# Optimization experiments

Hardware: AMD Instinct MI355X
Metric: run time of the kernel (lower is better)

The kernel has to match this reference:

```python
import jax, jax.numpy as jnp
import numpy as np

DN = ('NCHW', 'OIHW', 'NCHW')
PAD1 = [(1, 1), (1, 1)]


def conv3x3(x, w):
    return jax.lax.conv_general_dilated(x, w, window_strides=(1, 1), padding=PAD1, dimension_numbers=DN)


def setup_inputs() -> dict:
    key = jax.random.key(0)
    ks = jax.random.split(key, 5)
    B, C, H, W = 8, 256, 56, 56
    return {
        'x': jax.random.normal(ks[0], (B, C, H, W), jnp.float32),
        'weight': jax.random.normal(ks[1], (C, C, 3, 3), jnp.float32) * 0.05,
        'A_w': jax.random.normal(ks[2], (1, C, 3, 3), jnp.float32),
        'se_w1': jax.random.normal(ks[3], (16, C, 3, 3), jnp.float32) * 0.02,
        'se_w2': jax.random.normal(ks[4], (1, 16, 3, 3), jnp.float32) * 0.1,
    }


def reference(x, weight, A_w, se_w1, se_w2):
    # weight = weight * A_w (A_w broadcasts over the output-channel dim)
    w = weight * A_w  # [C, C, 3, 3]
    # SE-style spatial attention map A: [B, 1, H, W]
    a = jax.nn.sigmoid(conv3x3(jax.nn.relu(conv3x3(x, se_w1)), se_w2))
    # Torch: unfold(x) * A, then matmul with flattened weight. Since A
    # broadcasts across the C*9 patch dim, this equals conv2d(x, w) * A.
    out = conv3x3(x, w) * a  # [B, C, H, W]
    return out
```

## Files before the change

kernel.cpp:

```cpp
#include <hip/hip_runtime.h>


typedef unsigned short u16;
typedef __bf16 bf16x8 __attribute__((ext_vector_type(8)));
typedef unsigned short us8 __attribute__((ext_vector_type(8)));
typedef unsigned short us4v __attribute__((ext_vector_type(4)));
typedef float f32x4 __attribute__((ext_vector_type(4)));
typedef float f4v __attribute__((ext_vector_type(4)));

#define HP 58
#define HW 3136

__device__ __forceinline__ u16 f2bf(float f) {
  unsigned u = __float_as_uint(f);
  u = (u + 0x7fffu + ((u >> 16) & 1u)) >> 16;
  return (u16)u;
}
__device__ __forceinline__ float bf2f(u16 v) {
  return __uint_as_float(((unsigned)v) << 16);
}

__device__ __forceinline__ void gload16(const u16* g, u16* l) {
  __builtin_amdgcn_global_load_lds((const __attribute__((address_space(1))) void*)g,
                                   (__attribute__((address_space(3))) void*)l,
                                   16, 0, 0);
}

__global__ void k_prep(const float* __restrict__ weight, const float* __restrict__ A_w,
                       const float* __restrict__ se_w1, u16* __restrict__ wb,
                       u16* __restrict__ w1b) {
  int idx = blockIdx.x * 256 + threadIdx.x;
  if (idx < 589824) {
    int tap = idx >> 16; int rem = idx & 65535; int o = rem >> 8; int c = rem & 255;
    wb[idx] = f2bf(weight[(o * 256 + c) * 9 + tap] * A_w[c * 9 + tap]);
  } else if (idx < 589824 + 36864) {
    int j = idx - 589824;
    int tap = j >> 12; int rem = j & 4095; int o = rem >> 8; int c = rem & 255;
    w1b[j] = f2bf(se_w1[(o * 256 + c) * 9 + tap]);
  }
}

__global__ __launch_bounds__(256) void k_transform(const float* __restrict__ x,
                                                   u16* __restrict__ xp) {
  __shared__ __align__(16) u16 trans[56 * 72];
  const int t = threadIdx.x;
  const int h = blockIdx.x;
  const int b = blockIdx.y;
  for (int cc = 0; cc < 4; ++cc) {
    const int c0 = cc * 64;
#pragma unroll
    for (int i = 0; i < 4; ++i) {
      int idx = t + 256 * i;
      if (idx < 896) {
        int ci = idx / 14, s = idx % 14;
        f4v v = *(const f4v*)(x + ((size_t)(b * 256 + c0 + ci)) * HW + h * 56 + s * 4);
#pragma unroll
        for (int j = 0; j < 4; ++j) trans[(s * 4 + j) * 72 + ci] = f2bf(v[j]);
      }
    }
    __syncthreads();
#pragma unroll
    for (int i = 0; i < 2; ++i) {
      int idx = t + 256 * i;
      if (idx < 448) {
        int w = idx >> 3, seg = idx & 7;
        us8 v = *(const us8*)&trans[w * 72 + seg * 8];
        *(us8*)(xp + ((size_t)((b * HP + h + 1) * HP + (w + 1))) * 256 + c0 + seg * 8) = v;
      }
    }
    __syncthreads();
  }
}

__global__ __launch_bounds__(256) void k_se1(const u16* __restrict__ xp,
                                             const u16* __restrict__ w1b,
                                             u16* __restrict__ se1p) {
  __shared__ __align__(16) u16 Alds[144 * 8 * 8];
  __shared__ __align__(16) u16 slab[2080 * 8];
  const int t = threadIdx.x;
  const int lane = t & 63;
  const int wv = t >> 6;
  const int l15 = lane & 15, lg = lane >> 4;
  const int h0 = blockIdx.x * 2;
  const int b = blockIdx.y;

  f32x4 acc[2];
  f32x4 z = {0.f, 0.f, 0.f, 0.f};
  acc[0] = z; acc[1] = z;

  for (int cc = 0; cc < 4; ++cc) {
    const int c0 = cc * 64;
    __syncthreads();
    for (int idx = t; idx < 1152; idx += 256) {
      int row = idx >> 3, seg = idx & 7;
      us8 v = *(const us8*)(w1b + ((size_t)row * 256 + c0 + seg * 8));
      *(us8*)&Alds[(row * 8 + (seg ^ (row & 7))) * 8] = v;
    }
#pragma unroll
    for (int i = 0; i < 8; ++i) {
      int s_lin = wv * 512 + i * 64 + lane;
      int r = s_lin >> 9, col = (s_lin >> 3) & 63, seg = s_lin & 7;
      const u16* src = xp + ((size_t)((b * HP + h0 + r) * HP + col)) * 256 + c0 +
                       ((seg ^ (col & 7)) * 8);
      gload16(src, &slab[(wv * 512 + i * 64) * 8]);
    }
    __syncthreads();
    for (int dh = 0; dh < 3; ++dh) {
      for (int dw = 0; dw < 3; ++dw) {
        const int tap = dh * 3 + dw;
#pragma unroll
        for (int kk = 0; kk < 2; ++kk) {
          int arow = tap * 16 + l15;
          bf16x8 af = *(const bf16x8*)&Alds[(arow * 8 + ((kk * 4 + lg) ^ (arow & 7))) * 8];
#pragma unroll
          for (int nt = 0; nt < 2; ++nt) {
            int p = wv * 32 + nt * 16 + l15;
            int rr = (p >> 6) + dh, col = (p & 63) + dw;
            bf16x8 bfr = *(const bf16x8*)&slab[((rr * 64 + col) * 8 + ((kk * 4 + lg) ^ (col & 7))) * 8];
            acc[nt] = __builtin_amdgcn_mfma_f32_16x16x32_bf16(af, bfr, acc[nt], 0, 0, 0);
          }
        }
      }
    }
  }
#pragma unroll
  for (int nt = 0; nt < 2; ++nt) {
    int p = wv * 32 + nt * 16 + l15;
    int r = p >> 6, w = p & 63;
    if (w < 56) {
      us4v pk;
#pragma unroll
      for (int reg = 0; reg < 4; ++reg) {
        float v = acc[nt][reg];
        v = v > 0.f ? v : 0.f;
        pk[reg] = f2bf(v);
      }
      *(us4v*)(se1p + ((size_t)((b * HP + h0 + r + 1) * HP + (w + 1))) * 16 + lg * 4) = pk;
    }
  }
}

__global__ __launch_bounds__(256) void k_se2(const u16* __restrict__ se1p,
                                             const float* __restrict__ se_w2,
                                             float* __restrict__ amap) {
  __shared__ float w2s[144];
  const int t = threadIdx.x;
  for (int i = t; i < 144; i += 256) w2s[i] = se_w2[i];
  __syncthreads();
  int gid = blockIdx.x * 256 + t;
  int pix = gid >> 1, half = gid & 1;
  int b = pix / HW, p = pix % HW, h = p / 56, w = p % 56;
  float s = 0.f;
  for (int dh = 0; dh < 3; ++dh) {
#pragma unroll
    for (int dw = 0; dw < 3; ++dw) {
      const u16* src = se1p + ((size_t)((b * HP + h + dh) * HP + (w + dw))) * 16 + half * 8;
      us8 v = *(const us8*)src;
      int tap = dh * 3 + dw;
#pragma unroll
      for (int ci = 0; ci < 8; ++ci) s += bf2f(v[ci]) * w2s[(half * 8 + ci) * 9 + tap];
    }
  }
  s += __shfl_xor(s, 1);
  if (half == 0) amap[pix] = 1.f / (1.f + expf(-s));
}

__global__ __launch_bounds__(256) void k_main(const u16* __restrict__ xp,
                                              const u16* __restrict__ wb,
                                              const float* __restrict__ amap,
                                              float* __restrict__ out) {
  __shared__ __align__(16) u16 Alds[2][8192];
  __shared__ __align__(16) u16 Blds[2][8192];
  const int t = threadIdx.x;
  const int lane = t & 63;
  const int wid = t >> 6;
  const int wm = wid >> 1;
  const int wn = wid & 1;
  const int l15 = lane & 15, lg = lane >> 4;
  const int lrow = lane >> 3, lseg = lane & 7;
  const int mbase = blockIdx.x * 128;
  const int h0 = blockIdx.y * 2;
  const int b = blockIdx.z;

  f32x4 acc[4][4];
  f32x4 z = {0.f, 0.f, 0.f, 0.f};
#pragma unroll
  for (int mt = 0; mt < 4; ++mt)
#pragma unroll
    for (int nt = 0; nt < 4; ++nt) acc[mt][nt] = z;

  auto stage = [&](int buf, int it) {
    const int tap = it >> 2, cc = it & 3;
    const int dh = tap / 3, dw = tap % 3;
    const int c0 = cc * 64;
#pragma unroll
    for (int i = 0; i < 4; ++i) {
      int li = wid * 4 + i;
      int row = li * 8 + lrow;
      const u16* srcA = wb + ((size_t)(tap * 256 + mbase + row)) * 256 + c0 +
                        ((lseg ^ (row & 7)) * 8);
      gload16(srcA, &Alds[buf][li * 512]);
      int r = row >> 6, w = row & 63;
      const u16* srcB = xp +
                        ((size_t)((b * HP + h0 + r + dh) * HP + (w + dw))) * 256 + c0 +
                        ((lseg ^ (row & 7)) * 8);
      gload16(srcB, &Blds[buf][li * 512]);
    }
  };

  stage(0, 0);
#pragma unroll 2
  for (int it = 0; it < 36; ++it) {
    const int cur = it & 1;
    if (it < 35) {
      stage(cur ^ 1, it + 1);
      asm volatile("s_waitcnt vmcnt(8)" ::: "memory");
    } else {
      asm volatile("s_waitcnt vmcnt(0)" ::: "memory");
    }
    __builtin_amdgcn_s_barrier();
    __builtin_amdgcn_sched_barrier(0);
#pragma unroll
    for (int kk = 0; kk < 2; ++kk) {
      bf16x8 af[4], bfr[4];
#pragma unroll
      for (int mt = 0; mt < 4; ++mt) {
        int row = wm * 64 + mt * 16 + l15;
        af[mt] = *(const bf16x8*)&Alds[cur][row * 64 + (((kk * 4 + lg) ^ (row & 7)) * 8)];
      }
#pragma unroll
      for (int nt = 0; nt < 4; ++nt) {
        int p = wn * 64 + nt * 16 + l15;
        bfr[nt] = *(const bf16x8*)&Blds[cur][p * 64 + (((kk * 4 + lg) ^ (p & 7)) * 8)];
      }
#pragma unroll
      for (int mt = 0; mt < 4; ++mt)
#pragma unroll
        for (int nt = 0; nt < 4; ++nt)
          acc[mt][nt] = __builtin_amdgcn_mfma_f32_16x16x32_bf16(af[mt], bfr[nt], acc[mt][nt], 0, 0, 0);
    }
    __builtin_amdgcn_sched_barrier(0);
    __builtin_amdgcn_s_barrier();
  }
#pragma unroll
  for (int nt = 0; nt < 4; ++nt) {
    int n = wn * 64 + nt * 16 + l15;
    int r = n >> 6, w = n & 63;
    if (w < 56) {
      float av = amap[(b * 56 + h0 + r) * 56 + w];
#pragma unroll
      for (int mt = 0; mt < 4; ++mt) {
        int obase = mbase + wm * 64 + mt * 16 + lg * 4;
#pragma unroll
        for (int reg = 0; reg < 4; ++reg) {
          out[((size_t)(b * 256 + obase + reg) * 56 + h0 + r) * 56 + w] = acc[mt][nt][reg] * av;
        }
      }
    }
  }
}

extern "C" void kernel_launch(void* const* d_in, const int* in_sizes, int n_in,
                              void* d_out, int out_size, void* d_ws, size_t ws_size,
                              hipStream_t stream) {
  const float* x      = (const float*)d_in[0];
  const float* weight = (const float*)d_in[1];
  const float* A_w    = (const float*)d_in[2];
  const float* se_w1  = (const float*)d_in[3];
  const float* se_w2  = (const float*)d_in[4];
  float* out = (float*)d_out;

  char* ws = (char*)d_ws;
  u16* xp     = (u16*)ws;
  u16* se1p   = (u16*)(ws + 13778944);
  u16* wb     = (u16*)(ws + 14640128);
  u16* w1b    = (u16*)(ws + 15819776);
  float* amap = (float*)(ws + 15893504);

  hipMemsetAsync(ws, 0, 14640128, stream);
  k_prep<<<dim3((589824 + 36864 + 255) / 256), dim3(256), 0, stream>>>(weight, A_w, se_w1, wb, w1b);
  k_transform<<<dim3(56, 8), dim3(256), 0, stream>>>(x, xp);
  k_se1<<<dim3(28, 8), dim3(256), 0, stream>>>(xp, w1b, se1p);
  k_se2<<<dim3(196), dim3(256), 0, stream>>>(se1p, se_w2, amap);
  k_main<<<dim3(2, 28, 8), dim3(256), 0, stream>>>(xp, wb, amap, out);
}
```

Measured before the change: 154.3 us.

## Fuse prep kernels, stage input slab once per channel chunk, fold SE2 into main

New measurement: 171.4 us. 1.11x slower.

```diff
diff --git a/kernel.cpp b/kernel.cpp
--- a/kernel.cpp
+++ b/kernel.cpp
@@ -26,49 +26,73 @@
                                    16, 0, 0);
 }
 
-__global__ void k_prep(const float* __restrict__ weight, const float* __restrict__ A_w,
-                       const float* __restrict__ se_w1, u16* __restrict__ wb,
-                       u16* __restrict__ w1b) {
-  int idx = blockIdx.x * 256 + threadIdx.x;
-  if (idx < 589824) {
-    int tap = idx >> 16; int rem = idx & 65535; int o = rem >> 8; int c = rem & 255;
-    wb[idx] = f2bf(weight[(o * 256 + c) * 9 + tap] * A_w[c * 9 + tap]);
-  } else if (idx < 589824 + 36864) {
-    int j = idx - 589824;
-    int tap = j >> 12; int rem = j & 4095; int o = rem >> 8; int c = rem & 255;
-    w1b[j] = f2bf(se_w1[(o * 256 + c) * 9 + tap]);
-  }
-}
-
-__global__ __launch_bounds__(256) void k_transform(const float* __restrict__ x,
-                                                   u16* __restrict__ xp) {
+__global__ __launch_bounds__(256) void k_pre(const float* __restrict__ x,
+                                             const float* __restrict__ weight,
+                                             const float* __restrict__ A_w,
+                                             const float* __restrict__ se_w1,
+                                             u16* __restrict__ xp, u16* __restrict__ wb,
+                                             u16* __restrict__ w1b, u16* __restrict__ se1p) {
   __shared__ __align__(16) u16 trans[56 * 72];
+  const int bid = blockIdx.x;
   const int t = threadIdx.x;
-  const int h = blockIdx.x;
-  const int b = blockIdx.y;
-  for (int cc = 0; cc < 4; ++cc) {
-    const int c0 = cc * 64;
-#pragma unroll
-    for (int i = 0; i < 4; ++i) {
-      int idx = t + 256 * i;
-      if (idx < 896) {
-        int ci = idx / 14, s = idx % 14;
-        f4v v = *(const f4v*)(x + ((size_t)(b * 256 + c0 + ci)) * HW + h * 56 + s * 4);
-#pragma unroll
-        for (int j = 0; j < 4; ++j) trans[(s * 4 + j) * 72 + ci] = f2bf(v[j]);
-      }
-    }
-    __syncthreads();
-#pragma unroll
-    for (int i = 0; i < 2; ++i) {
-      int idx = t + 256 * i;
-      if (idx < 448) {
-        int w = idx >> 3, seg = idx & 7;
-        us8 v = *(const us8*)&trans[w * 72 + seg * 8];
-        *(us8*)(xp + ((size_t)((b * HP + h + 1) * HP + (w + 1))) * 256 + c0 + seg * 8) = v;
-      }
-    }
-    __syncthreads();
+  if (bid < 448) {
+    const int h = bid % 56, b = bid / 56;
+    if (t < 64) {
+      int half = t >> 5, seg = t & 31;
+      us8 z8 = {};
+      *(us8*)(xp + ((size_t)((b * HP + h + 1) * HP + half * 57)) * 256 + seg * 8) = z8;
+    }
+    for (int cc = 0; cc < 4; ++cc) {
+      const int c0 = cc * 64;
+#pragma unroll
+      for (int i = 0; i < 4; ++i) {
+        int idx = t + 256 * i;
+        if (idx < 896) {
+          int ci = idx / 14, s = idx % 14;
+          f4v v = *(const f4v*)(x + ((size_t)(b * 256 + c0 + ci)) * HW + h * 56 + s * 4);
+#pragma unroll
+          for (int j = 0; j < 4; ++j) trans[(s * 4 + j) * 72 + ci] = f2bf(v[j]);
+        }
+      }
+      __syncthreads();
+#pragma unroll
+      for (int i = 0; i < 2; ++i) {
+        int idx = t + 256 * i;
+        if (idx < 448) {
+          int w = idx >> 3, seg = idx & 7;
+          us8 v = *(const us8*)&trans[w * 72 + seg * 8];
+          *(us8*)(xp + ((size_t)((b * HP + h + 1) * HP + (w + 1))) * 256 + c0 + seg * 8) = v;
+        }
+      }
+      __syncthreads();
+    }
+  } else if (bid < 2896) {
+    int idx = (bid - 448) * 256 + t;
+    if (idx < 589824) {
+      int tap = idx >> 16; int rem = idx & 65535; int o = rem >> 8; int c = rem & 255;
+      wb[idx] = f2bf(weight[(o * 256 + c) * 9 + tap] * A_w[c * 9 + tap]);
+    } else if (idx < 589824 + 36864) {
+      int j = idx - 589824;
+      int tap = j >> 12; int rem = j & 4095; int o = rem >> 8; int c = rem & 255;
+      w1b[j] = f2bf(se_w1[(o * 256 + c) * 9 + tap]);
+    }
+  } else {
+    int zid = (bid - 2896) * 256 + t;
+    us8 z8 = {};
+#pragma unroll
+    for (int j = 0; j < 2; ++j) {
+      int ch = zid + j * 45056;
+      if (ch < 29696) {
+        int b = ch / 3712; int rem = ch - b * 3712;
+        int row = (rem < 1856) ? 0 : 57;
+        int r2 = (rem < 1856) ? rem : rem - 1856;
+        int col = r2 >> 5, seg = r2 & 31;
+        *(us8*)(xp + ((size_t)((b * HP + row) * HP + col)) * 256 + seg * 8) = z8;
+      } else if (ch < 29696 + 53824) {
+        int c2 = ch - 29696;
+        *(us8*)(se1p + (size_t)c2 * 8) = z8;
+      }
+    }
   }
 }
 
@@ -81,8 +105,9 @@
   const int lane = t & 63;
   const int wv = t >> 6;
   const int l15 = lane & 15, lg = lane >> 4;
-  const int h0 = blockIdx.x * 2;
-  const int b = blockIdx.y;
+  const int wg = blockIdx.x;
+  const int b = wg & 7;
+  const int h0 = (wg >> 3) * 2;
 
   f32x4 acc[2];
   f32x4 z = {0.f, 0.f, 0.f, 0.f};
@@ -140,37 +165,15 @@
   }
 }
 
-__global__ __launch_bounds__(256) void k_se2(const u16* __restrict__ se1p,
-                                             const float* __restrict__ se_w2,
-                                             float* __restrict__ amap) {
-  __shared__ float w2s[144];
-  const int t = threadIdx.x;
-  for (int i = t; i < 144; i += 256) w2s[i] = se_w2[i];
-  __syncthreads();
-  int gid = blockIdx.x * 256 + t;
-  int pix = gid >> 1, half = gid & 1;
-  int b = pix / HW, p = pix % HW, h = p / 56, w = p % 56;
-  float s = 0.f;
-  for (int dh = 0; dh < 3; ++dh) {
-#pragma unroll
-    for (int dw = 0; dw < 3; ++dw) {
-      const u16* src = se1p + ((size_t)((b * HP + h + dh) * HP + (w + dw))) * 16 + half * 8;
-      us8 v = *(const us8*)src;
-      int tap = dh * 3 + dw;
-#pragma unroll
-      for (int ci = 0; ci < 8; ++ci) s += bf2f(v[ci]) * w2s[(half * 8 + ci) * 9 + tap];
-    }
-  }
-  s += __shfl_xor(s, 1);
-  if (half == 0) amap[pix] = 1.f / (1.f + expf(-s));
-}
-
 __global__ __launch_bounds__(256) void k_main(const u16* __restrict__ xp,
                                               const u16* __restrict__ wb,
-                                              const float* __restrict__ amap,
+                                              const u16* __restrict__ se1p,
+                                              const float* __restrict__ se_w2,
                                               float* __restrict__ out) {
-  __shared__ __align__(16) u16 Alds[2][8192];
-  __shared__ __align__(16) u16 Blds[2][8192];
+  __shared__ __align__(16) u16 slab[4 * 64 * 8 * 8];
+  __shared__ __align__(16) u16 Albuf[2][128 * 64];
+  __shared__ float w2s[144];
+  __shared__ float amap_s[128];
   const int t = threadIdx.x;
   const int lane = t & 63;
   const int wid = t >> 6;
@@ -178,9 +181,13 @@
   const int wn = wid & 1;
   const int l15 = lane & 15, lg = lane >> 4;
   const int lrow = lane >> 3, lseg = lane & 7;
-  const int mbase = blockIdx.x * 128;
-  const int h0 = blockIdx.y * 2;
-  const int b = blockIdx.z;
+  const int wg = blockIdx.x;
+  const int b = wg & 7;
+  const int rem = wg >> 3;
+  const int h0 = (rem >> 1) * 2;
+  const int mbase = (rem & 1) * 128;
+
+  if (t < 144) w2s[t] = se_w2[t];
 
   f32x4 acc[4][4];
   f32x4 z = {0.f, 0.f, 0.f, 0.f};
@@ -189,65 +196,100 @@
 #pragma unroll
     for (int nt = 0; nt < 4; ++nt) acc[mt][nt] = z;
 
-  auto stage = [&](int buf, int it) {
-    const int tap = it >> 2, cc = it & 3;
-    const int dh = tap / 3, dw = tap % 3;
+  auto stage_slab = [&](int cc) {
+    const int c0 = cc * 64;
+#pragma unroll
+    for (int i = 0; i < 8; ++i) {
+      int chunk = wid * 512 + i * 64 + lane;
+      int row = chunk >> 9, col = (chunk >> 3) & 63, seg = chunk & 7;
+      const u16* src = xp + ((size_t)((b * HP + h0 + row) * HP + col)) * 256 + c0 +
+                       ((seg ^ (col & 7)) * 8);
+      gload16(src, &slab[(wid * 512 + i * 64) * 8]);
+    }
+  };
+  auto stage_A = [&](int tap, int cc, int buf) {
     const int c0 = cc * 64;
 #pragma unroll
     for (int i = 0; i < 4; ++i) {
       int li = wid * 4 + i;
       int row = li * 8 + lrow;
-      const u16* srcA = wb + ((size_t)(tap * 256 + mbase + row)) * 256 + c0 +
-                        ((lseg ^ (row & 7)) * 8);
-      gload16(srcA, &Alds[buf][li * 512]);
-      int r = row >> 6, w = row & 63;
-      const u16* srcB = xp +
-                        ((size_t)((b * HP + h0 + r + dh) * HP + (w + dw))) * 256 + c0 +
-                        ((lseg ^ (row & 7)) * 8);
-      gload16(srcB, &Blds[buf][li * 512]);
+      const u16* src = wb + ((size_t)(tap * 256 + mbase + row)) * 256 + c0 +
+                       ((lseg ^ (row & 7)) * 8);
+      gload16(src, &Albuf[buf][li * 512]);
     }
   };
 
-  stage(0, 0);
-#pragma unroll 2
-  for (int it = 0; it < 36; ++it) {
-    const int cur = it & 1;
-    if (it < 35) {
-      stage(cur ^ 1, it + 1);
-      asm volatile("s_waitcnt vmcnt(8)" ::: "memory");
-    } else {
-      asm volatile("s_waitcnt vmcnt(0)" ::: "memory");
-    }
-    __builtin_amdgcn_s_barrier();
-    __builtin_amdgcn_sched_barrier(0);
-#pragma unroll
-    for (int kk = 0; kk < 2; ++kk) {
-      bf16x8 af[4], bfr[4];
-#pragma unroll
-      for (int mt = 0; mt < 4; ++mt) {
-        int row = wm * 64 + mt * 16 + l15;
-        af[mt] = *(const bf16x8*)&Alds[cur][row * 64 + (((kk * 4 + lg) ^ (row & 7)) * 8)];
-      }
-#pragma unroll
-      for (int nt = 0; nt < 4; ++nt) {
-        int p = wn * 64 + nt * 16 + l15;
-        bfr[nt] = *(const bf16x8*)&Blds[cur][p * 64 + (((kk * 4 + lg) ^ (p & 7)) * 8)];
-      }
-#pragma unroll
-      for (int mt = 0; mt < 4; ++mt)
-#pragma unroll
-        for (int nt = 0; nt < 4; ++nt)
-          acc[mt][nt] = __builtin_amdgcn_mfma_f32_16x16x32_bf16(af[mt], bfr[nt], acc[mt][nt], 0, 0, 0);
-    }
-    __builtin_amdgcn_sched_barrier(0);
-    __builtin_amdgcn_s_barrier();
-  }
+  stage_slab(0);
+  stage_A(0, 0, 0);
+  int pb = 0;
+  for (int cc = 0; cc < 4; ++cc) {
+    for (int tap = 0; tap < 9; ++tap) {
+      if (tap < 8) {
+        stage_A(tap + 1, cc, pb ^ 1);
+        asm volatile("s_waitcnt vmcnt(4)" ::: "memory");
+      } else {
+        asm volatile("s_waitcnt vmcnt(0)" ::: "memory");
+      }
+      __builtin_amdgcn_s_barrier();
+      __builtin_amdgcn_sched_barrier(0);
+      const int dh = tap / 3, dw = tap % 3;
+#pragma unroll
+      for (int kk = 0; kk < 2; ++kk) {
+        bf16x8 af[4], bfr[4];
+#pragma unroll
+        for (int mt = 0; mt < 4; ++mt) {
+          int row = wm * 64 + mt * 16 + l15;
+          af[mt] = *(const bf16x8*)&Albuf[pb][row * 64 + (((kk * 4 + lg) ^ (row & 7)) * 8)];
+        }
+#pragma unroll
+        for (int nt = 0; nt < 4; ++nt) {
+          int p = wn * 64 + nt * 16 + l15;
+          int r = (p >> 6) + dh;
+          int col = ((p & 63) + dw) & 63;
+          bfr[nt] = *(const bf16x8*)&slab[((r * 64 + col) * 8 + ((kk * 4 + lg) ^ (col & 7))) * 8];
+        }
+#pragma unroll
+        for (int mt = 0; mt < 4; ++mt)
+#pragma unroll
+          for (int nt = 0; nt < 4; ++nt)
+            acc[mt][nt] = __builtin_amdgcn_mfma_f32_16x16x32_bf16(af[mt], bfr[nt], acc[mt][nt], 0, 0, 0);
+      }
+      __builtin_amdgcn_sched_barrier(0);
+      __builtin_amdgcn_s_barrier();
+      if (tap < 8) {
+        pb ^= 1;
+      } else if (cc < 3) {
+        stage_slab(cc + 1);
+        stage_A(0, cc + 1, pb);
+      }
+    }
+  }
+  if (t < 112) {
+    int r = t / 56, w = t - r * 56;
+    int h = h0 + r;
+    float s = 0.f;
+    for (int dh2 = 0; dh2 < 3; ++dh2) {
+#pragma unroll
+      for (int dw2 = 0; dw2 < 3; ++dw2) {
+        const u16* src = se1p + ((size_t)((b * HP + h + dh2) * HP + (w + dw2))) * 16;
+        us8 v0 = *(const us8*)src;
+        us8 v1 = *(const us8*)(src + 8);
+        int tap = dh2 * 3 + dw2;
+#pragma unroll
+        for (int ci = 0; ci < 8; ++ci) s += bf2f(v0[ci]) * w2s[ci * 9 + tap];
+#pragma unroll
+        for (int ci = 0; ci < 8; ++ci) s += bf2f(v1[ci]) * w2s[(8 + ci) * 9 + tap];
+      }
+    }
+    amap_s[t] = 1.f / (1.f + expf(-s));
+  }
+  __syncthreads();
 #pragma unroll
   for (int nt = 0; nt < 4; ++nt) {
     int n = wn * 64 + nt * 16 + l15;
     int r = n >> 6, w = n & 63;
     if (w < 56) {
-      float av = amap[(b * 56 + h0 + r) * 56 + w];
+      float av = amap_s[r * 56 + w];
 #pragma unroll
       for (int mt = 0; mt < 4; ++mt) {
         int obase = mbase + wm * 64 + mt * 16 + lg * 4;
@@ -271,16 +313,12 @@
   float* out = (float*)d_out;
 
   char* ws = (char*)d_ws;
-  u16* xp     = (u16*)ws;
-  u16* se1p   = (u16*)(ws + 13778944);
-  u16* wb     = (u16*)(ws + 14640128);
-  u16* w1b    = (u16*)(ws + 15819776);
-  float* amap = (float*)(ws + 15893504);
-
-  hipMemsetAsync(ws, 0, 14640128, stream);
-  k_prep<<<dim3((589824 + 36864 + 255) / 256), dim3(256), 0, stream>>>(weight, A_w, se_w1, wb, w1b);
-  k_transform<<<dim3(56, 8), dim3(256), 0, stream>>>(x, xp);
-  k_se1<<<dim3(28, 8), dim3(256), 0, stream>>>(xp, w1b, se1p);
-  k_se2<<<dim3(196), dim3(256), 0, stream>>>(se1p, se_w2, amap);
-  k_main<<<dim3(2, 28, 8), dim3(256), 0, stream>>>(xp, wb, amap, out);
-}
+  u16* xp   = (u16*)ws;
+  u16* se1p = (u16*)(ws + 13778944);
+  u16* wb   = (u16*)(ws + 14640128);
+  u16* w1b  = (u16*)(ws + 15819776);
+
+  k_pre<<<dim3(3072), dim3(256), 0, stream>>>(x, weight, A_w, se_w1, xp, wb, w1b, se1p);
+  k_se1<<<dim3(224), dim3(256), 0, stream>>>(xp, w1b, se1p);
+  k_main<<<dim3(448), dim3(256), 0, stream>>>(xp, wb, se1p, se_w2, out);
+}
```
